# Performance work log

Measured on AMD Instinct MI355X. Metric: run time of the kernel, lower is better.

The kernel has to match this reference:

```python
import jax, jax.numpy as jnp
import numpy as np

NEG = -9e10


def _gat_layer(h_in, adj_mask, W, a, alpha, concat):
    # h_in: [N, Fin], W: [Fin, Fout], a: [2*Fout, 1]
    h = h_in @ W                                  # [N, Fout]
    Fout = W.shape[1]
    a1 = a[:Fout, 0]                              # [Fout]
    a2 = a[Fout:, 0]                              # [Fout]
    # e[i,j] = leakyrelu(h_i . a1 + h_j . a2)  (decomposed repeat+cat score)
    s1 = h @ a1                                   # [N]
    s2 = h @ a2                                   # [N]
    e = jax.nn.leaky_relu(s1[:, None] + s2[None, :], negative_slope=alpha)  # [N, N]
    e = jnp.where(adj_mask, e, NEG)
    att = jax.nn.softmax(e, axis=1)               # [N, N]
    h_prime = att @ h                             # [N, Fout]
    return jax.nn.elu(h_prime) if concat else h_prime


def setup_inputs() -> dict:
    key = jax.random.key(0)
    ks = jax.random.split(key, 6)
    N, nfeat, nhid, nheads, nout = 4096, 512, 64, 8, 56
    x = jax.random.normal(ks[0], (N, nfeat), dtype=jnp.float32)
    adj = jax.random.randint(ks[1], (N, N), 0, 2, dtype=jnp.int32)
    Ws = jax.random.normal(ks[2], (nheads, nfeat, nhid), dtype=jnp.float32) * 0.05
    As = jax.random.normal(ks[3], (nheads, 2 * nhid, 1), dtype=jnp.float32) * 0.05
    W_out = jax.random.normal(ks[4], (nhid, nout), dtype=jnp.float32) * 0.05
    a_out = jax.random.normal(ks[5], (2 * nout, 1), dtype=jnp.float32) * 0.05
    return {"x": x, "adj": adj, "Ws": Ws, "As": As, "W_out": W_out, "a_out": a_out}


def reference(x, adj, Ws, As, W_out, a_out):
    alpha = 0.2
    nheads = Ws.shape[0]
    adj_mask = adj > 0
    # dropout is identity in eval mode
    heads = jax.vmap(lambda W, a: _gat_layer(x, adj_mask, W, a, alpha, True))(Ws, As)
    z = jnp.sum(heads, axis=0) / nheads           # [N, nhid] (heads averaged, per source)
    out = _gat_layer(z, adj_mask, W_out, a_out, alpha, False)
    out = jax.nn.elu(out)                         # [N, 56]
    return jax.nn.softmax(out, axis=1)
```

## Files before the change

### kernel.cpp

```cpp
#include <hip/hip_runtime.h>
#include <hip/hip_bf16.h>
#include <math.h>


#define GN 4096
#define GNH 8
#define LOG2E 1.4426950408889634f

typedef __bf16 bf16x8 __attribute__((ext_vector_type(8)));
typedef float f32x4 __attribute__((ext_vector_type(4)));

#if defined(__has_builtin)
#if __has_builtin(__builtin_amdgcn_exp2f)
#define FAST_EXP2(x) __builtin_amdgcn_exp2f(x)
#endif
#if __has_builtin(__builtin_amdgcn_perm)
#define FAST_PERM(a, b, s) __builtin_amdgcn_perm((a), (b), (s))
#endif
#endif
#ifndef FAST_EXP2
#define FAST_EXP2(x) __expf((x)*0.6931471805599453f)
#endif
#ifndef FAST_PERM
__device__ inline unsigned FAST_PERM(unsigned a, unsigned b, unsigned) {
    return (a & 0xFFFF0000u) | (b >> 16);
}
#endif

__device__ inline unsigned hi_pack2(float w0, float w1) {
    unsigned u0 = __float_as_uint(w0) + 0x8000u;
    unsigned u1 = __float_as_uint(w1) + 0x8000u;
    return FAST_PERM(u1, u0, 0x07060302u);
}

__global__ __launch_bounds__(256) void prep(const int* __restrict__ adj,
                                            const float* __restrict__ x,
                                            const float* __restrict__ Ws,
                                            unsigned long long* __restrict__ adjb,
                                            unsigned short* __restrict__ xh,
                                            unsigned short* __restrict__ wth) {
    const int b = blockIdx.x;
    const int tid = threadIdx.x;
    if (b < 16384) {
        const int wv = tid >> 6, lane = tid & 63;
        const size_t ebase = ((size_t)b * 4 + wv) * 256;
        unsigned long long m[4];
        #pragma unroll
        for (int e = 0; e < 4; ++e)
            m[e] = __ballot(adj[ebase + e * 64 + lane] > 0);
        if (lane == 0) {
            #pragma unroll
            for (int e = 0; e < 4; ++e) adjb[(ebase >> 6) + e] = m[e];
        }
    } else if (b < 17408) {
        int gid = (b - 16384) * 256 + tid;
        int i = gid >> 6, c64 = gid & 63;
        const float* xp = x + (size_t)i * 512 + c64 * 8;
        float4 a = *(const float4*)xp;
        float4 v = *(const float4*)(xp + 4);
        unsigned hp[4];
        hp[0] = hi_pack2(a.x, a.y);
        hp[1] = hi_pack2(a.z, a.w);
        hp[2] = hi_pack2(v.x, v.y);
        hp[3] = hi_pack2(v.z, v.w);
        int il = i & 63, kt = c64 >> 3, c = c64 & 7;
        size_t base = ((size_t)(i >> 6) * 8 + kt) * 4096 + il * 64 + ((c ^ (il & 7)) * 8);
        *(uint4*)&xh[base] = *(uint4*)hp;
    } else {
        __shared__ float t[64][65];
        int b2 = b - 17408;
        int head = b2 >> 3, k0 = (b2 & 7) * 64;
        #pragma unroll
        for (int it = 0; it < 4; ++it) {
            int e = (tid + it * 256) * 4;
            int kl = e >> 6, f4 = e & 63;
            float4 v = *(const float4*)&Ws[((size_t)head * 512 + k0 + kl) * 64 + f4];
            t[f4 + 0][kl] = v.x; t[f4 + 1][kl] = v.y;
            t[f4 + 2][kl] = v.z; t[f4 + 3][kl] = v.w;
        }
        __syncthreads();
        int f = tid >> 2;
        #pragma unroll
        for (int p = 0; p < 2; ++p) {
            int c = (tid & 3) * 2 + p;
            unsigned hp[4];
            #pragma unroll
            for (int pp = 0; pp < 4; ++pp)
                hp[pp] = hi_pack2(t[f][c * 8 + 2 * pp], t[f][c * 8 + 2 * pp + 1]);
            size_t base = (size_t)b2 * 4096 + f * 64 + ((c ^ (f & 7)) * 8);
            *(uint4*)&wth[base] = *(uint4*)hp;
        }
    }
}

__global__ __launch_bounds__(256) void gemm_fused(const unsigned short* __restrict__ xh,
                                                  const unsigned short* __restrict__ wth,
                                                  const float* __restrict__ As,
                                                  unsigned short* __restrict__ imgh,
                                                  float* __restrict__ rL,
                                                  float2* __restrict__ ebL) {
    __shared__ __align__(16) unsigned short lds[2][2][4096];
    const int tid = threadIdx.x;
    const int head = blockIdx.x;
    const int itile = blockIdx.y;
    const int i0 = itile * 64;
    const unsigned short* srcs[2] = {xh + (size_t)itile * 8 * 4096,
                                     wth + (size_t)head * 8 * 4096};
    const int lane = tid & 63, wv_ = tid >> 6;
    const int mi = (wv_ & 1) * 32, fi = (wv_ >> 1) * 32;
    const int row = lane & 15, quad = lane >> 4;
    f32x4 acc[2][2] = {};

    #define GSTAGE(buf, kt)                                                                \
        do {                                                                               \
            _Pragma("unroll")                                                              \
            for (int q_ = 0; q_ < 2; ++q_) {                                               \
                const unsigned short* s_ = srcs[q_] + (size_t)(kt) * 4096;                 \
                _Pragma("unroll")                                                          \
                for (int c_ = 0; c_ < 2; ++c_)                                             \
                    __builtin_amdgcn_global_load_lds(                                      \
                        (const __attribute__((address_space(1))) unsigned int*)(s_ + c_ * 2048 + tid * 8), \
                        (__attribute__((address_space(3))) unsigned int*)&lds[buf][q_][c_ * 2048 + tid * 8], \
                        16, 0, 0);                                                         \
            }                                                                              \
        } while (0)

    GSTAGE(0, 0);
    for (int kt = 0; kt < 8; ++kt) {
        __syncthreads();
        const int cur = kt & 1;
        if (kt + 1 < 8) GSTAGE(cur ^ 1, kt + 1);
        #pragma unroll
        for (int ks = 0; ks < 2; ++ks) {
            bf16x8 ah[2], bh[2];
            #pragma unroll
            for (int t = 0; t < 2; ++t) {
                const int m_ = mi + t * 16 + row;
                const int offa = m_ * 64 + (((ks * 4 + quad) ^ (m_ & 7)) * 8);
                ah[t] = *(const bf16x8*)&lds[cur][0][offa];
                const int f_ = fi + t * 16 + row;
                const int offb = f_ * 64 + (((ks * 4 + quad) ^ (f_ & 7)) * 8);
                bh[t] = *(const bf16x8*)&lds[cur][1][offb];
            }
            #pragma unroll
            for (int mt = 0; mt < 2; ++mt)
                #pragma unroll
                for (int nt = 0; nt < 2; ++nt)
                    acc[mt][nt] = __builtin_amdgcn_mfma_f32_16x16x32_bf16(ah[mt], bh[nt], acc[mt][nt], 0, 0, 0);
        }
    }
    #undef GSTAGE
    __syncthreads();
    float* ht = (float*)&lds[0][0][0];
    #pragma unroll
    for (int mt = 0; mt < 2; ++mt)
        #pragma unroll
        for (int nt = 0; nt < 2; ++nt)
            #pragma unroll
            for (int r = 0; r < 4; ++r)
                ht[(mi + mt * 16 + quad * 4 + r) * 68 + fi + nt * 16 + row] = acc[mt][nt][r];
    __syncthreads();
    {
        const int rrow = tid >> 2, seg = (tid & 3) * 16;
        const float* ah = As + head * 128;
        float p1 = 0.f, p2 = 0.f;
        #pragma unroll
        for (int c = 0; c < 16; ++c) {
            float v = ht[rrow * 68 + seg + c];
            p1 += v * ah[seg + c];
            p2 += v * ah[64 + seg + c];
        }
        p1 += __shfl_xor(p1, 1); p1 += __shfl_xor(p1, 2);
        p2 += __shfl_xor(p2, 1); p2 += __shfl_xor(p2, 2);
        if ((tid & 3) == 0) {
            const int gi = i0 + rrow;
            rL[head * GN + gi] = FAST_EXP2(0.8f * p1 * LOG2E);
            float2 e;
            e.x = FAST_EXP2(p2 * LOG2E);
            e.y = FAST_EXP2(0.2f * p2 * LOG2E);
            ebL[head * GN + gi] = e;
        }
    }
    {
        const int f = tid >> 2;
        size_t base = ((size_t)head * 64 + itile) * 4096 + (size_t)f * 64;
        #pragma unroll
        for (int p = 0; p < 2; ++p) {
            int c = (tid & 3) * 2 + p;
            unsigned hp[4];
            #pragma unroll
            for (int pp = 0; pp < 4; ++pp)
                hp[pp] = hi_pack2(ht[(c * 8 + 2 * pp) * 68 + f], ht[(c * 8 + 2 * pp + 1) * 68 + f]);
            int off = (c ^ (f & 7)) * 8;
            *(uint4*)&imgh[base + off] = *(uint4*)hp;
        }
    }
}

template <int NCHUNK>
__global__ __launch_bounds__(256, 4) void attn10(const unsigned short* __restrict__ imgh,
                                                 const float* __restrict__ rg,
                                                 const float2* __restrict__ ebg,
                                                 const unsigned long long* __restrict__ adjb,
                                                 float* __restrict__ pO,
                                                 float* __restrict__ pd) {
    __shared__ __align__(16) unsigned short hb[2][4096];
    const int tid = threadIdx.x;
    const int lane = tid & 63, wv = tid >> 6;
    const int row = lane & 15, quad = lane >> 4;
    const int head = blockIdx.y / NCHUNK;
    const int chunk = blockIdx.y % NCHUNK;
    const int i0 = blockIdx.x * 64;
    const int jb = chunk * (GN / NCHUNK);
    const int njt = (GN / NCHUNK) / 64;
    const int jt0 = jb >> 6;
    const unsigned short* ih = imgh + (size_t)head * (64 * GN);
    const float2* ebh = ebg + (size_t)head * GN;
    const int gr = i0 + wv * 16 + row;
    const float rv = rg[head * GN + gr];
    const unsigned long long* adjr = adjb + (size_t)gr * 64 + jt0;

    f32x4 acc[4] = {};
    float den = 0.f;

    #define STAGE(buf, T)                                                                  \
        do {                                                                               \
            const unsigned short* gh_ = ih + (size_t)(T) * 4096;                           \
            _Pragma("unroll")                                                              \
            for (int c_ = 0; c_ < 2; ++c_)                                                 \
                __builtin_amdgcn_global_load_lds(                                          \
                    (const __attribute__((address_space(1))) unsigned int*)(gh_ + c_ * 2048 + tid * 8), \
                    (__attribute__((address_space(3))) unsigned int*)&hb[buf][c_ * 2048 + tid * 8],     \
                    16, 0, 0);                                                             \
        } while (0)

    STAGE(0, jt0);
    for (int jt = 0; jt < njt; ++jt) {
        __syncthreads();
        const int cur = jt & 1;
        const int j0 = jb + jt * 64;
        const unsigned long long wd = adjr[jt];
        const float4* ep0 = (const float4*)(ebh + j0 + quad * 8);
        const float4* ep1 = (const float4*)(ebh + j0 + 32 + quad * 8);
        const float4 f00 = ep0[0], f01 = ep0[1], f02 = ep0[2], f03 = ep0[3];
        const float4 f10 = ep1[0], f11 = ep1[1], f12 = ep1[2], f13 = ep1[3];
        if (jt + 1 < njt) STAGE(cur ^ 1, jt0 + jt + 1);
        #pragma unroll
        for (int ks = 0; ks < 2; ++ks) {
            const int kb = ks * 32 + quad * 8;
            const unsigned bits = (unsigned)(wd >> kb) & 0xFFu;
            const float4 e4[4] = {ks ? f10 : f00, ks ? f11 : f01,
                                  ks ? f12 : f02, ks ? f13 : f03};
            union { unsigned u[4]; bf16x8 v; } hfr;
            #pragma unroll
            for (int p = 0; p < 4; ++p) {
                const float4 e = e4[p];
                const float m0 = (float)((bits >> (2 * p)) & 1u);
                const float m1 = (float)((bits >> (2 * p + 1)) & 1u);
                const float w0 = fmaxf(rv * e.x, e.y) * m0;
                const float w1 = fmaxf(rv * e.z, e.w) * m1;
                unsigned u0 = __float_as_uint(w0) + 0x8000u;
                unsigned u1 = __float_as_uint(w1) + 0x8000u;
                den += __uint_as_float(u0 & 0xFFFF0000u) + __uint_as_float(u1 & 0xFFFF0000u);
                hfr.u[p] = FAST_PERM(u1, u0, 0x07060302u);
            }
            #pragma unroll
            for (int nt = 0; nt < 4; ++nt) {
                const int f = nt * 16 + row;
                const int off = f * 64 + (((ks * 4 + quad) ^ (f & 7)) * 8);
                bf16x8 bh = *(const bf16x8*)&hb[cur][off];
                acc[nt] = __builtin_amdgcn_mfma_f32_16x16x32_bf16(hfr.v, bh, acc[nt], 0, 0, 0);
            }
        }
    }
    #undef STAGE
    den += __shfl_xor(den, 16);
    den += __shfl_xor(den, 32);
    float* o = pO + (size_t)blockIdx.y * (GN * 64);
    #pragma unroll
    for (int r = 0; r < 4; ++r) {
        const int grow = i0 + wv * 16 + quad * 4 + r;
        #pragma unroll
        for (int nt = 0; nt < 4; ++nt)
            o[(size_t)grow * 64 + nt * 16 + row] = acc[nt][r];
    }
    if (lane < 16) pd[blockIdx.y * GN + i0 + wv * 16 + lane] = den;
}

__global__ __launch_bounds__(256) void mid(const float* __restrict__ pO,
                                           const float* __restrict__ pd,
                                           const float* __restrict__ Wo,
                                           const float* __restrict__ ao,
                                           unsigned short* __restrict__ img2h,
                                           float* __restrict__ rbL,
                                           float2* __restrict__ eb2L) {
    __shared__ __align__(16) float zt[16][68];
    __shared__ float Wl[64 * 57];
    __shared__ float invd[8][16];
    const int tid = threadIdx.x;
    const int i0 = blockIdx.x * 16;
    for (int idx = tid; idx < 64 * 56; idx += 256) {
        int k = idx / 56, c = idx - k * 56;
        Wl[k * 57 + c] = Wo[idx];
    }
    if (tid < 128) {
        int hd = tid >> 4, r = tid & 15;
        invd[hd][r] = 1.f / (pd[(2 * hd) * GN + i0 + r] + pd[(2 * hd + 1) * GN + i0 + r]);
    }
    __syncthreads();
    #pragma unroll
    for (int it = 0; it < 4; ++it) {
        int e = it * 256 + tid;
        int r = e >> 6, f = e & 63;
        size_t base = (size_t)(i0 + r) * 64 + f;
        float s = 0.f;
        #pragma unroll
        for (int hd = 0; hd < GNH; ++hd) {
            float o = pO[(size_t)(2 * hd) * (GN * 64) + base] +
                      pO[(size_t)(2 * hd + 1) * (GN * 64) + base];
            float v = o * invd[hd][r];
            s += v > 0.f ? v : FAST_EXP2(v * LOG2E) - 1.f;
        }
        zt[r][f] = s * 0.125f;
    }
    __syncthreads();
    const int rrow = tid >> 4, cseg = (tid & 15) * 4;
    float hreg[4] = {0.f, 0.f, 0.f, 0.f};
    for (int k0 = 0; k0 < 64; k0 += 4) {
        float4 zv = *(const float4*)&zt[rrow][k0];
        #pragma unroll
        for (int c = 0; c < 4; ++c) {
            int col = cseg + c;
            if (col < 56)
                hreg[c] += zv.x * Wl[k0 * 57 + col] + zv.y * Wl[(k0 + 1) * 57 + col] +
                           zv.z * Wl[(k0 + 2) * 57 + col] + zv.w * Wl[(k0 + 3) * 57 + col];
        }
    }
    {
        float p1 = 0.f, p2 = 0.f;
        #pragma unroll
        for (int c = 0; c < 4; ++c) {
            int col = cseg + c;
            if (col < 56) {
                p1 += hreg[c] * ao[col];
                p2 += hreg[c] * ao[56 + col];
            }
        }
        p1 += __shfl_xor(p1, 1); p1 += __shfl_xor(p1, 2);
        p1 += __shfl_xor(p1, 4); p1 += __shfl_xor(p1, 8);
        p2 += __shfl_xor(p2, 1); p2 += __shfl_xor(p2, 2);
        p2 += __shfl_xor(p2, 4); p2 += __shfl_xor(p2, 8);
        if ((tid & 15) == 0) {
            rbL[i0 + rrow] = FAST_EXP2(0.8f * p1 * LOG2E);
            float2 e;
            e.x = FAST_EXP2(p2 * LOG2E);
            e.y = FAST_EXP2(0.2f * p2 * LOG2E);
            eb2L[i0 + rrow] = e;
        }
    }
    __syncthreads();
    #pragma unroll
    for (int c = 0; c < 4; ++c) zt[rrow][cseg + c] = (cseg + c < 56) ? hreg[c] : 0.f;
    __syncthreads();
    if (tid < 128) {
        const int jt = i0 >> 6;
        const int cbase = (i0 & 63) >> 3;
        const int f = tid >> 1, c = cbase + (tid & 1);
        const int lr = (tid & 1) * 8;
        unsigned hp[4];
        #pragma unroll
        for (int pp = 0; pp < 4; ++pp)
            hp[pp] = hi_pack2(zt[lr + 2 * pp][f], zt[lr + 2 * pp + 1][f]);
        size_t base = (size_t)jt * 4096 + f * 64 + ((c ^ (f & 7)) * 8);
        *(uint4*)&img2h[base] = *(uint4*)hp;
    }
}

__global__ __launch_bounds__(256) void fink2(const float* __restrict__ pO,
                                             const float* __restrict__ pd,
                                             float* __restrict__ out) {
    const int lane = threadIdx.x & 63;
    const int w = threadIdx.x >> 6;
    const int i = blockIdx.x * 4 + w;
    float o = 0.f, d = 0.f;
    #pragma unroll
    for (int c = 0; c < 16; ++c) d += pd[c * GN + i];
    if (lane < 56) {
        #pragma unroll
        for (int c = 0; c < 16; ++c) o += pO[(size_t)c * (GN * 64) + (size_t)i * 64 + lane];
    }
    float v = -1e30f;
    if (lane < 56) {
        float t = o / d;
        v = t > 0.f ? t : expm1f(t);
    }
    float m = v;
    #pragma unroll
    for (int off = 32; off; off >>= 1) m = fmaxf(m, __shfl_down(m, off));
    m = __shfl(m, 0);
    float p = (lane < 56) ? __expf(v - m) : 0.f;
    float s = p;
    #pragma unroll
    for (int off = 32; off; off >>= 1) s += __shfl_down(s, off);
    s = __shfl(s, 0);
    if (lane < 56) out[(size_t)i * 56 + lane] = p / s;
}

extern "C" void kernel_launch(void* const* d_in, const int* in_sizes, int n_in,
                              void* d_out, int out_size, void* d_ws, size_t ws_size,
                              hipStream_t stream) {
    const float* x    = (const float*)d_in[0];
    const int*   adj  = (const int*)d_in[1];
    const float* Ws   = (const float*)d_in[2];
    const float* As   = (const float*)d_in[3];
    const float* Wo   = (const float*)d_in[4];
    const float* ao   = (const float*)d_in[5];
    float* out = (float*)d_out;

    char* ws = (char*)d_ws;
    unsigned long long* adjb = (unsigned long long*)(ws + 0);
    unsigned short* img1h = (unsigned short*)(ws + 2097152);
    float* pO    = (float*)(ws + 6291456);
    unsigned short* x_hi = (unsigned short*)(ws + 6291456);
    float* pd    = (float*)(ws + 23068672);
    float* rL    = (float*)(ws + 23330816);
    float2* ebL  = (float2*)(ws + 23461888);
    float* rbL   = (float*)(ws + 23724032);
    float2* eb2L = (float2*)(ws + 23740416);
    unsigned short* img2h = (unsigned short*)(ws + 23773184);
    unsigned short* WT_hi = (unsigned short*)(ws + 24297472);

    prep<<<17472, 256, 0, stream>>>(adj, x, Ws, adjb, x_hi, WT_hi);
    gemm_fused<<<dim3(8, 64), 256, 0, stream>>>(x_hi, WT_hi, As, img1h, rL, ebL);
    attn10<2><<<dim3(64, 16), 256, 0, stream>>>(img1h, rL, ebL, adjb, pO, pd);
    mid<<<256, 256, 0, stream>>>(pO, pd, Wo, ao, img2h, rbL, eb2L);
    attn10<16><<<dim3(64, 16), 256, 0, stream>>>(img2h, rbL, eb2L, adjb, pO, pd);
    fink2<<<1024, 256, 0, stream>>>(pO, pd, out);
}
```

Measured before the change: 215.5 us.

## Load attention B-fragments directly from global in MFMA-native layout, drop LDS staging

The producer kernels now write the bf16 h image in an MFMA fragment-native layout, so the attention kernel loads each B operand with one coalesced 16-byte global load per lane instead of staging through double-buffered LDS with barriers. The softmax denominator is now computed by an extra MFMA against a ones vector rather than scalar adds, and the next tile's score vectors and adjacency word are prefetched in registers. This removes __syncthreads and LDS traffic, at the cost of redundant global/L2 reads across the four waves and more register pressure.

```diff
diff --git a/kernel.cpp b/kernel.cpp
--- a/kernel.cpp
+++ b/kernel.cpp
@@ -183,7 +183,7 @@
     }
     {
         const int f = tid >> 2;
-        size_t base = ((size_t)head * 64 + itile) * 4096 + (size_t)f * 64;
+        size_t base = ((size_t)head * 64 + itile) * 4096;
         #pragma unroll
         for (int p = 0; p < 2; ++p) {
             int c = (tid & 3) * 2 + p;
@@ -191,20 +191,20 @@
             #pragma unroll
             for (int pp = 0; pp < 4; ++pp)
                 hp[pp] = hi_pack2(ht[(c * 8 + 2 * pp) * 68 + f], ht[(c * 8 + 2 * pp + 1) * 68 + f]);
-            int off = (c ^ (f & 7)) * 8;
+            size_t off = (size_t)(c >> 2) * 2048 + (size_t)(f >> 4) * 512 +
+                         (size_t)((c & 3) * 16 + (f & 15)) * 8;
             *(uint4*)&imgh[base + off] = *(uint4*)hp;
         }
     }
 }
 
 template <int NCHUNK>
-__global__ __launch_bounds__(256, 4) void attn10(const unsigned short* __restrict__ imgh,
+__global__ __launch_bounds__(256, 4) void attn11(const unsigned short* __restrict__ imgh,
                                                  const float* __restrict__ rg,
                                                  const float2* __restrict__ ebg,
                                                  const unsigned long long* __restrict__ adjb,
                                                  float* __restrict__ pO,
                                                  float* __restrict__ pd) {
-    __shared__ __align__(16) unsigned short hb[2][4096];
     const int tid = threadIdx.x;
     const int lane = tid & 63, wv = tid >> 6;
     const int row = lane & 15, quad = lane >> 4;
@@ -221,61 +221,65 @@
     const unsigned long long* adjr = adjb + (size_t)gr * 64 + jt0;
 
     f32x4 acc[4] = {};
-    float den = 0.f;
-
-    #define STAGE(buf, T)                                                                  \
+    f32x4 accd = {};
+    union { unsigned u[4]; bf16x8 v; } ones;
+    #pragma unroll
+    for (int q = 0; q < 4; ++q) ones.u[q] = 0x3F803F80u;
+
+    const char* tbl = (const char*)(ih + (size_t)jt0 * 4096) + lane * 16;
+    const float4* ebq = (const float4*)ebh + (jb >> 1) + quad * 4;
+
+    #define KS(WD, KSC, E0, E1, E2, E3, Q0, Q1, Q2, Q3)                                    \
         do {                                                                               \
-            const unsigned short* gh_ = ih + (size_t)(T) * 4096;                           \
+            const unsigned bits = (unsigned)((WD) >> ((KSC) * 32 + quad * 8)) & 0xFFu;     \
+            const float4 ee[4] = {E0, E1, E2, E3};                                         \
+            union { unsigned u[4]; bf16x8 v; } wfr;                                        \
             _Pragma("unroll")                                                              \
-            for (int c_ = 0; c_ < 2; ++c_)                                                 \
-                __builtin_amdgcn_global_load_lds(                                          \
-                    (const __attribute__((address_space(1))) unsigned int*)(gh_ + c_ * 2048 + tid * 8), \
-                    (__attribute__((address_space(3))) unsigned int*)&hb[buf][c_ * 2048 + tid * 8],     \
-                    16, 0, 0);                                                             \
+            for (int p = 0; p < 4; ++p) {                                                  \
+                const float4 e = ee[p];                              \
+                const float m0 = (float)((bits >> (2 * p)) & 1u);                          \
+                const float m1 = (float)((bits >> (2 * p + 1)) & 1u);                      \
+                const float w0 = fmaxf(rv * e.x, e.y) * m0;                                \
+                const float w1 = fmaxf(rv * e.z, e.w) * m1;                                \
+                wfr.u[p] = hi_pack2(w0, w1);                                               \
+            }                                                                              \
+            accd = __builtin_amdgcn_mfma_f32_16x16x32_bf16(wfr.v, ones.v, accd, 0, 0, 0);  \
+            union { uint4 q; bf16x8 v; } b0u, b1u, b2u, b3u;                               \
+            b0u.q = Q0; b1u.q = Q1; b2u.q = Q2; b3u.q = Q3;                                \
+            acc[0] = __builtin_amdgcn_mfma_f32_16x16x32_bf16(wfr.v, b0u.v, acc[0], 0, 0, 0); \
+            acc[1] = __builtin_amdgcn_mfma_f32_16x16x32_bf16(wfr.v, b1u.v, acc[1], 0, 0, 0); \
+            acc[2] = __builtin_amdgcn_mfma_f32_16x16x32_bf16(wfr.v, b2u.v, acc[2], 0, 0, 0); \
+            acc[3] = __builtin_amdgcn_mfma_f32_16x16x32_bf16(wfr.v, b3u.v, acc[3], 0, 0, 0); \
         } while (0)
 
-    STAGE(0, jt0);
+    float4 n0 = ebq[0], n1 = ebq[1], n2 = ebq[2], n3 = ebq[3];
+    unsigned long long wdn = adjr[0];
+
+    #pragma unroll 2
     for (int jt = 0; jt < njt; ++jt) {
-        __syncthreads();
-        const int cur = jt & 1;
-        const int j0 = jb + jt * 64;
-        const unsigned long long wd = adjr[jt];
-        const float4* ep0 = (const float4*)(ebh + j0 + quad * 8);
-        const float4* ep1 = (const float4*)(ebh + j0 + 32 + quad * 8);
-        const float4 f00 = ep0[0], f01 = ep0[1], f02 = ep0[2], f03 = ep0[3];
-        const float4 f10 = ep1[0], f11 = ep1[1], f12 = ep1[2], f13 = ep1[3];
-        if (jt + 1 < njt) STAGE(cur ^ 1, jt0 + jt + 1);
-        #pragma unroll
-        for (int ks = 0; ks < 2; ++ks) {
-            const int kb = ks * 32 + quad * 8;
-            const unsigned bits = (unsigned)(wd >> kb) & 0xFFu;
-            const float4 e4[4] = {ks ? f10 : f00, ks ? f11 : f01,
-                                  ks ? f12 : f02, ks ? f13 : f03};
-            union { unsigned u[4]; bf16x8 v; } hfr;
-            #pragma unroll
-            for (int p = 0; p < 4; ++p) {
-                const float4 e = e4[p];
-                const float m0 = (float)((bits >> (2 * p)) & 1u);
-                const float m1 = (float)((bits >> (2 * p + 1)) & 1u);
-                const float w0 = fmaxf(rv * e.x, e.y) * m0;
-                const float w1 = fmaxf(rv * e.z, e.w) * m1;
-                unsigned u0 = __float_as_uint(w0) + 0x8000u;
-                unsigned u1 = __float_as_uint(w1) + 0x8000u;
-                den += __uint_as_float(u0 & 0xFFFF0000u) + __uint_as_float(u1 & 0xFFFF0000u);
-                hfr.u[p] = FAST_PERM(u1, u0, 0x07060302u);
-            }
-            #pragma unroll
-            for (int nt = 0; nt < 4; ++nt) {
-                const int f = nt * 16 + row;
-                const int off = f * 64 + (((ks * 4 + quad) ^ (f & 7)) * 8);
-                bf16x8 bh = *(const bf16x8*)&hb[cur][off];
-                acc[nt] = __builtin_amdgcn_mfma_f32_16x16x32_bf16(hfr.v, bh, acc[nt], 0, 0, 0);
-            }
-        }
-    }
-    #undef STAGE
-    den += __shfl_xor(den, 16);
-    den += __shfl_xor(den, 32);
+        const float4 f0 = n0, f1 = n1, f2 = n2, f3 = n3;
+        const unsigned long long wd = wdn;
+        const uint4 q0 = *(const uint4*)(tbl + 0);
+        const uint4 q1 = *(const uint4*)(tbl + 1024);
+        const uint4 q2 = *(const uint4*)(tbl + 2048);
+        const uint4 q3 = *(const uint4*)(tbl + 3072);
+        const uint4 q4 = *(const uint4*)(tbl + 4096);
+        const uint4 q5 = *(const uint4*)(tbl + 5120);
+        const uint4 q6 = *(const uint4*)(tbl + 6144);
+        const uint4 q7 = *(const uint4*)(tbl + 7168);
+        const float4* e1 = ebq + jt * 32 + 16;
+        const float4 c0 = e1[0], c1 = e1[1], c2 = e1[2], c3 = e1[3];
+        if (jt + 1 < njt) {
+            const float4* e0 = ebq + (jt + 1) * 32;
+            n0 = e0[0]; n1 = e0[1]; n2 = e0[2]; n3 = e0[3];
+            wdn = adjr[jt + 1];
+        }
+        KS(wd, 0, f0, f1, f2, f3, q0, q1, q2, q3);
+        KS(wd, 1, c0, c1, c2, c3, q4, q5, q6, q7);
+        tbl += 8192;
+    }
+    #undef KS
+
     float* o = pO + (size_t)blockIdx.y * (GN * 64);
     #pragma unroll
     for (int r = 0; r < 4; ++r) {
@@ -284,7 +288,11 @@
         for (int nt = 0; nt < 4; ++nt)
             o[(size_t)grow * 64 + nt * 16 + row] = acc[nt][r];
     }
-    if (lane < 16) pd[blockIdx.y * GN + i0 + wv * 16 + lane] = den;
+    if (row == 0) {
+        #pragma unroll
+        for (int r = 0; r < 4; ++r)
+            pd[blockIdx.y * GN + i0 + wv * 16 + quad * 4 + r] = accd[r];
+    }
 }
 
 __global__ __launch_bounds__(256) void mid(const float* __restrict__ pO,
@@ -371,7 +379,8 @@
         #pragma unroll
         for (int pp = 0; pp < 4; ++pp)
             hp[pp] = hi_pack2(zt[lr + 2 * pp][f], zt[lr + 2 * pp + 1][f]);
-        size_t base = (size_t)jt * 4096 + f * 64 + ((c ^ (f & 7)) * 8);
+        size_t base = (size_t)jt * 4096 + (size_t)(c >> 2) * 2048 +
+                      (size_t)(f >> 4) * 512 + (size_t)((c & 3) * 16 + (f & 15)) * 8;
         *(uint4*)&img2h[base] = *(uint4*)hp;
     }
 }
@@ -432,8 +441,8 @@
 
     prep<<<17472, 256, 0, stream>>>(adj, x, Ws, adjb, x_hi, WT_hi);
     gemm_fused<<<dim3(8, 64), 256, 0, stream>>>(x_hi, WT_hi, As, img1h, rL, ebL);
-    attn10<2><<<dim3(64, 16), 256, 0, stream>>>(img1h, rL, ebL, adjb, pO, pd);
+    attn11<2><<<dim3(64, 16), 256, 0, stream>>>(img1h, rL, ebL, adjb, pO, pd);
     mid<<<256, 256, 0, stream>>>(pO, pd, Wo, ao, img2h, rbL, eb2L);
-    attn10<16><<<dim3(64, 16), 256, 0, stream>>>(img2h, rbL, eb2L, adjb, pO, pd);
+    attn11<16><<<dim3(64, 16), 256, 0, stream>>>(img2h, rbL, eb2L, adjb, pO, pd);
     fink2<<<1024, 256, 0, stream>>>(pO, pd, out);
 }
```

Measured after the change: 231.3 us. 1.07x slower.
